# Kernel optimization log

Measured on AMD Instinct MI355X. Metric: run time of the kernel, lower is better.

## Reference

```python
import jax, jax.numpy as jnp
import numpy as np

T, B = 16, 32
C, H, W = 3, 120, 160
NET, LSTM_H, AC_H, NACT = 512, 512, 512, 8
CONV_OUT = 64 * 11 * 16  # 11264, from 120x160 through k[8,4,3]/s[4,2,1]


def setup_inputs() -> dict:
    key = jax.random.key(0)
    ks = jax.random.split(key, 32)
    rn = lambda k, shape, s=0.05: jax.random.normal(k, shape, jnp.float32) * s
    return {
        "x": jax.random.normal(ks[0], (T * B, C, H, W), jnp.float32),
        "done": jax.random.randint(ks[1], (T * B,), 0, 2, jnp.int32),
        "h0": rn(ks[2], (1, B, LSTM_H), 1.0),
        "c0": rn(ks[3], (1, B, LSTM_H), 1.0),
        "w1": rn(ks[4], (32, C, 8, 8)), "b1": jnp.zeros((32,), jnp.float32),
        "w2": rn(ks[5], (64, 32, 4, 4)), "b2": jnp.zeros((64,), jnp.float32),
        "w3": rn(ks[6], (64, 64, 3, 3)), "b3": jnp.zeros((64,), jnp.float32),
        "fcW": rn(ks[7], (NET, CONV_OUT), 0.01), "fcb": jnp.zeros((NET,), jnp.float32),
        "Wih": rn(ks[8], (4 * LSTM_H, NET)), "Whh": rn(ks[9], (4 * LSTM_H, LSTM_H)),
        "bih": jnp.zeros((4 * LSTM_H,), jnp.float32), "bhh": jnp.zeros((4 * LSTM_H,), jnp.float32),
        "A1": rn(ks[10], (AC_H, LSTM_H)), "Ab1": jnp.zeros((AC_H,), jnp.float32),
        "A2": rn(ks[11], (NACT, AC_H)), "Ab2": jnp.zeros((NACT,), jnp.float32),
        "C1": rn(ks[12], (AC_H, LSTM_H)), "Cb1": jnp.zeros((AC_H,), jnp.float32),
        "C2": rn(ks[13], (1, AC_H)), "Cb2": jnp.zeros((1,), jnp.float32),
    }


DN = ("NCHW", "OIHW", "NCHW")


def _conv(x, w, b, s):
    y = jax.lax.conv_general_dilated(x, w, (s, s), "VALID", dimension_numbers=DN)
    return y + b[None, :, None, None]


def reference(x, done, h0, c0, w1, b1, w2, b2, w3, b3, fcW, fcb,
              Wih, Whh, bih, bhh, A1, Ab1, A2, Ab2, C1, Cb1, C2, Cb2):
    # CNN feature extractor
    h = jax.nn.relu(_conv(x, w1, b1, 4))
    h = jax.nn.relu(_conv(h, w2, b2, 2))
    h = jax.nn.relu(_conv(h, w3, b3, 1))
    h = h.reshape(h.shape[0], -1)                     # [T*B, CONV_OUT]
    h = jax.nn.leaky_relu(h @ fcW.T + fcb, 0.2)       # [T*B, NET]

    bsz = h0.shape[1]
    xs = h.reshape(-1, bsz, Wih.shape[1])             # [T, B, NET]
    d = done.astype(h.dtype).reshape(-1, bsz)         # [T, B]

    def step(carry, inp):
        hs, cs = carry
        xt, dt = inp
        m = (1.0 - dt)[:, None]                       # done-mask reset
        hs, cs = hs * m, cs * m
        g = xt @ Wih.T + bih + hs @ Whh.T + bhh       # [B, 4H], gate order i,f,g,o
        i, f, gg, o = jnp.split(g, 4, axis=-1)
        cs = jax.nn.sigmoid(f) * cs + jax.nn.sigmoid(i) * jnp.tanh(gg)
        hs = jax.nn.sigmoid(o) * jnp.tanh(cs)
        return (hs, cs), hs

    (hT, cT), outs = jax.lax.scan(step, (h0[0], c0[0]), (xs, d))
    nh = outs.reshape(-1, outs.shape[-1])             # [T*B, LSTM_H]

    a = jax.nn.leaky_relu(nh @ A1.T + Ab1, 0.01)
    logits = a @ A2.T + Ab2                           # [T*B, NACT]
    v = jax.nn.leaky_relu(nh @ C1.T + Cb1, 0.01)
    value = v @ C2.T + Cb2                            # [T*B, 1]
    return logits, value, hT[None], cT[None]
```

## Files before the change

### kernel.cpp

```cpp
#include <hip/hip_runtime.h>
#include <hip/hip_bf16.h>
#include <math.h>

using short8 = __attribute__((ext_vector_type(8))) short;
using f32x4  = __attribute__((ext_vector_type(4))) float;
typedef unsigned long long u64;

#define MFMA16(a, b, c) __builtin_amdgcn_mfma_f32_16x16x32_bf16(a, b, c, 0, 0, 0)

__device__ __forceinline__ short f2bs(float f) {
    __hip_bfloat16 h = __float2bfloat16(f);
    return __builtin_bit_cast(short, h);
}
__device__ __forceinline__ float bs2f(short s) {
    return __uint_as_float(((unsigned)(unsigned short)s) << 16);
}

__global__ void __launch_bounds__(256) k_megaprep(
        const float* __restrict__ w1, const float* __restrict__ w2,
        const float* __restrict__ w3, const float* __restrict__ fcW,
        const float* __restrict__ Wih, const float* __restrict__ Whh,
        const float* __restrict__ A1, const float* __restrict__ C1,
        const float* __restrict__ A2, const float* __restrict__ C2,
        const float* __restrict__ h0, const int* __restrict__ done,
        const float* __restrict__ bih, const float* __restrict__ bhh,
        const float* __restrict__ Ab1, const float* __restrict__ Cb1,
        short* __restrict__ wc1, short* __restrict__ wc2, short* __restrict__ wc3,
        short* __restrict__ fcwr, short* __restrict__ wihb, short* __restrict__ whhb,
        short* __restrict__ a1b, short* __restrict__ c1b, short* __restrict__ a2b,
        short* __restrict__ c2b, short* __restrict__ hm0,
        float* __restrict__ bias2, float* __restrict__ biasAC, unsigned* __restrict__ flags) {
    __shared__ short t[176 * 76];
    const int bid = blockIdx.x, tid = threadIdx.x;

    auto cvt4 = [&](const float* in, short* out, int i) {
        float4 v = *(const float4*)(in + i * 4);
        out[i * 4 + 0] = f2bs(v.x); out[i * 4 + 1] = f2bs(v.y);
        out[i * 4 + 2] = f2bs(v.z); out[i * 4 + 3] = f2bs(v.w);
    };

    if (bid < 512) {
        int r = bid;
        for (int it = 0; it < 11; ++it) {
            int c4 = it * 256 + tid;
            float4 v = *(const float4*)(fcW + (size_t)r * 11264 + c4 * 4);
            int c = c4 * 4;
            int oc = c / 176, pix = c % 176;
            t[(pix + 0) * 76 + oc] = f2bs(v.x);
            t[(pix + 1) * 76 + oc] = f2bs(v.y);
            t[(pix + 2) * 76 + oc] = f2bs(v.z);
            t[(pix + 3) * 76 + oc] = f2bs(v.w);
        }
        __syncthreads();
        for (int it = 0; it < 6; ++it) {
            int j8 = it * 256 + tid;
            if (j8 < 1408) {
                int j = j8 * 8, pix = j >> 6, oc0 = j & 63;
                const short* tp = &t[pix * 76 + oc0];
                short8 v;
                ((uint2*)&v)[0] = *(const uint2*)tp;
                ((uint2*)&v)[1] = *(const uint2*)(tp + 4);
                *(short8*)&fcwr[(size_t)r * 11264 + j] = v;
            }
        }
    } else if (bid < 1536) {
        cvt4(Wih, wihb, (bid - 512) * 256 + tid);
    } else if (bid < 2560) {
        cvt4(Whh, whhb, (bid - 1536) * 256 + tid);
    } else if (bid < 2816) {
        cvt4(A1, a1b, (bid - 2560) * 256 + tid);
    } else if (bid < 3072) {
        cvt4(C1, c1b, (bid - 2816) * 256 + tid);
    } else if (bid < 3078) {
        cvt4(w1, wc1, (bid - 3072) * 256 + tid);
    } else if (bid < 3206) {
        int i = (bid - 3078) * 256 + tid;
        int oc = i >> 9, col = i & 511;
        int kh = col >> 7, kw = (col >> 5) & 3, ic = col & 31;
        wc2[i] = f2bs(w2[((oc * 32 + ic) * 4 + kh) * 4 + kw]);
    } else if (bid < 3350) {
        int i = (bid - 3206) * 256 + tid;
        int oc = i / 576, col = i % 576;
        int kh = col / 192, r = col % 192, kw = r >> 6, ic = r & 63;
        wc3[i] = f2bs(w3[((oc * 64 + ic) * 3 + kh) * 3 + kw]);
    } else if (bid < 3354) {
        cvt4(A2, a2b, (bid - 3350) * 256 + tid);
    } else if (bid < 3355) {
        if (tid < 128) cvt4(C2, c2b, tid);
    } else if (bid < 3419) {
        int i = (bid - 3355) * 256 + tid;
        float m = 1.f - (float)done[i >> 9];
        hm0[i] = f2bs(h0[i] * m);
    } else if (bid < 3427) {
        int i = (bid - 3419) * 256 + tid;
        bias2[i] = bih[i] + bhh[i];
    } else if (bid < 3431) {
        int i = (bid - 3427) * 256 + tid;
        biasAC[i] = (i < 512) ? Ab1[i] : Cb1[i - 512];
    } else {
        if (tid < 16) flags[tid] = 0u;
    }
}

__global__ void __launch_bounds__(256) k_conv1_v4(const float* __restrict__ x,
                                                  const short* __restrict__ Wc,
                                                  const float* __restrict__ bias,
                                                  short* __restrict__ y) {
    __shared__ short ct[4][512];
    const int tid = threadIdx.x;
    const int w = tid >> 6, l = tid & 63;
    const int lr = l & 15, lg = l >> 4;
    short8 bf[6][2];
#pragma unroll
    for (int ks = 0; ks < 6; ++ks)
#pragma unroll
        for (int nf = 0; nf < 2; ++nf)
            bf[ks][nf] = *(const short8*)&Wc[(nf * 16 + lr) * 192 + ks * 32 + lg * 8];
    const float bc0 = bias[lr], bc1 = bias[16 + lr];
    const int t0 = blockIdx.x * 16 + w * 4;

    auto mkbase = [&](int t) -> const float* {
        unsigned m = (unsigned)(t * 16 + lr);
        unsigned n = m / 1131u, pix = m % 1131u;
        unsigned oh = pix / 39u, ow = pix - oh * 39u;
        return x + (size_t)n * 57600 + (oh * 4) * 160 + ow * 4;
    };

    float4 fA[6][2], fB[6][2];
    {
        const float* base = mkbase(t0);
#pragma unroll
        for (int ks = 0; ks < 6; ++ks) {
            int ic = ks >> 1, kh = (ks & 1) * 4 + lg;
            const float* ap = base + ic * 19200 + kh * 160;
            fA[ks][0] = *(const float4*)ap;
            fA[ks][1] = *(const float4*)(ap + 4);
        }
    }
#pragma unroll
    for (int i = 0; i < 4; ++i) {
        const int t = t0 + i;
        if (i < 3) {
            const float* nb = mkbase(t + 1);
#pragma unroll
            for (int ks = 0; ks < 6; ++ks) {
                int ic = ks >> 1, kh = (ks & 1) * 4 + lg;
                const float* ap = nb + ic * 19200 + kh * 160;
                fB[ks][0] = *(const float4*)ap;
                fB[ks][1] = *(const float4*)(ap + 4);
            }
        }
        f32x4 acc[2] = {};
#pragma unroll
        for (int ks = 0; ks < 6; ++ks) {
            short8 a;
            a[0] = f2bs(fA[ks][0].x); a[1] = f2bs(fA[ks][0].y);
            a[2] = f2bs(fA[ks][0].z); a[3] = f2bs(fA[ks][0].w);
            a[4] = f2bs(fA[ks][1].x); a[5] = f2bs(fA[ks][1].y);
            a[6] = f2bs(fA[ks][1].z); a[7] = f2bs(fA[ks][1].w);
            acc[0] = MFMA16(a, bf[ks][0], acc[0]);
            acc[1] = MFMA16(a, bf[ks][1], acc[1]);
        }
#pragma unroll
        for (int j = 0; j < 4; ++j) {
            ct[w][(lg * 4 + j) * 32 + lr] = f2bs(fmaxf(acc[0][j] + bc0, 0.f));
            ct[w][(lg * 4 + j) * 32 + 16 + lr] = f2bs(fmaxf(acc[1][j] + bc1, 0.f));
        }
        asm volatile("s_waitcnt lgkmcnt(0)" ::: "memory");
        int row = l >> 2, c8 = (l & 3) * 8;
        short8 v = *(const short8*)&ct[w][row * 32 + c8];
        *(short8*)&y[((size_t)t * 16 + row) * 32 + c8] = v;
        asm volatile("s_waitcnt lgkmcnt(0)" ::: "memory");
        if (i < 3) {
#pragma unroll
            for (int ks = 0; ks < 6; ++ks) {
                fA[ks][0] = fB[ks][0];
                fA[ks][1] = fB[ks][1];
            }
        }
    }
}

__global__ void __launch_bounds__(256) k_conv23(const short* __restrict__ a1,
                                                const short* __restrict__ Wc2,
                                                const float* __restrict__ b2,
                                                const short* __restrict__ Wc3,
                                                const float* __restrict__ b3,
                                                short* __restrict__ y3) {
    __shared__ short img1[36192];
    __shared__ short img2[14976];
    __shared__ short ct[2][1024];
    const int n = blockIdx.x, tid = threadIdx.x;
    const int w = tid >> 6, l = tid & 63, lr = l & 15, lg = l >> 4;
    const int par = w >> 1, nfh = w & 1;

    {
        short8 bfg[16][2];
#pragma unroll
        for (int ks = 0; ks < 16; ++ks)
#pragma unroll
            for (int q2 = 0; q2 < 2; ++q2)
                bfg[ks][q2] = *(const short8*)&Wc2[(nfh * 32 + q2 * 16 + lr) * 512 + ks * 32 + lg * 8];
        float bc[2] = {b2[nfh * 32 + lr], b2[nfh * 32 + 16 + lr]};
        const short* src = a1 + (size_t)n * 36192;
        for (int it = 0; it < 18; ++it) {
            int i8 = it * 256 + tid;
            if (i8 < 4524) {
                short8 v = *(const short8*)(src + i8 * 8);
                int b = i8 * 16;
                b ^= ((b >> 7) & 7) << 4;
                *(short8*)((char*)img1 + b) = v;
            }
        }
        __syncthreads();
        for (int t = par; t < 16; t += 2) {
            int p = t * 16 + lr;
            int pc = p < 234 ? p : 233;
            int oh = pc / 18, ow = pc - oh * 18;
            int base = (oh * 2 * 39 + ow * 2) * 64 + lg * 16;
            f32x4 acc[2] = {};
#pragma unroll
            for (int ks = 0; ks < 16; ++ks) {
                int kh = ks >> 2, kw = ks & 3;
                int b = base + (kh * 39 + kw) * 64;
                b ^= ((b >> 7) & 7) << 4;
                short8 a = *(const short8*)((const char*)img1 + b);
                acc[0] = MFMA16(a, bfg[ks][0], acc[0]);
                acc[1] = MFMA16(a, bfg[ks][1], acc[1]);
            }
#pragma unroll
            for (int q2 = 0; q2 < 2; ++q2)
#pragma unroll
                for (int j = 0; j < 4; ++j)
                    ct[par][(lg * 4 + j) * 64 + nfh * 32 + q2 * 16 + lr] =
                        f2bs(fmaxf(acc[q2][j] + bc[q2], 0.f));
            __syncthreads();
            int li = nfh * 64 + l;
            int row = li >> 3, c8 = (li & 7) * 8;
            short8 v = *(const short8*)&ct[par][row * 64 + c8];
            int pg = t * 16 + row;
            if (pg < 234) {
                int b = (pg * 64 + c8) * 2;
                b ^= ((b >> 7) & 7) << 4;
                *(short8*)((char*)img2 + b) = v;
            }
            __syncthreads();
        }
    }
    __syncthreads();

    {
        short8 bfg[18][2];
#pragma unroll
        for (int ks = 0; ks < 18; ++ks)
#pragma unroll
            for (int q2 = 0; q2 < 2; ++q2)
                bfg[ks][q2] = *(const short8*)&Wc3[(nfh * 32 + q2 * 16 + lr) * 576 + ks * 32 + lg * 8];
        float bc[2] = {b3[nfh * 32 + lr], b3[nfh * 32 + 16 + lr]};
        for (int t = par; t < 12; t += 2) {
            int p = t * 16 + lr;
            int pc = p < 176 ? p : 175;
            int oh = pc >> 4, ow = pc & 15;
            int base = (oh * 18 + ow) * 128 + lg * 16;
            f32x4 acc[2] = {};
#pragma unroll
            for (int ks = 0; ks < 18; ++ks) {
                int kh = ks / 6, r6 = ks % 6, kw = r6 >> 1, ich = r6 & 1;
                int b = base + (kh * 18 + kw) * 128 + ich * 64;
                b ^= ((b >> 7) & 7) << 4;
                short8 a = *(const short8*)((const char*)img2 + b);
                acc[0] = MFMA16(a, bfg[ks][0], acc[0]);
                acc[1] = MFMA16(a, bfg[ks][1], acc[1]);
            }
#pragma unroll
            for (int q2 = 0; q2 < 2; ++q2)
#pragma unroll
                for (int j = 0; j < 4; ++j)
                    ct[par][(lg * 4 + j) * 64 + nfh * 32 + q2 * 16 + lr] =
                        f2bs(fmaxf(acc[q2][j] + bc[q2], 0.f));
            __syncthreads();
            int li = nfh * 64 + l;
            int row = li >> 3, c8 = (li & 7) * 8;
            short8 v = *(const short8*)&ct[par][row * 64 + c8];
            int pg = t * 16 + row;
            if (pg < 176)
                *(short8*)&y3[((size_t)n * 176 + pg) * 64 + c8] = v;
            __syncthreads();
        }
    }
}

__global__ void k_gemm_mfma(const short* __restrict__ A, const short* __restrict__ W,
                            float* __restrict__ part, int M, int N, int K, int kPerSplit) {
    __shared__ short As[2][64 * 40];
    __shared__ short Ws[2][64 * 40];
    const int tid = threadIdx.x;
    const int m0 = blockIdx.y * 64, n0 = blockIdx.x * 64;
    const int k0s = blockIdx.z * kPerSplit, k0e = k0s + kPerSplit;
    const int w = tid >> 6, l = tid & 63;
    const int wr = w >> 1, wc = w & 1;
    const int sr = tid >> 2, sc = tid & 3;
    const int lr = l & 15, lg = l >> 4;
    f32x4 acc[2][2] = {};
    for (int k0 = k0s; k0 < k0e; k0 += 64) {
        short8 av0 = *(const short8*)(A + (size_t)(m0 + sr) * K + k0 + sc * 8);
        short8 av1 = *(const short8*)(A + (size_t)(m0 + sr) * K + k0 + 32 + sc * 8);
        short8 wv0 = *(const short8*)(W + (size_t)(n0 + sr) * K + k0 + sc * 8);
        short8 wv1 = *(const short8*)(W + (size_t)(n0 + sr) * K + k0 + 32 + sc * 8);
        __syncthreads();
        *(short8*)&As[0][sr * 40 + sc * 8] = av0;
        *(short8*)&As[1][sr * 40 + sc * 8] = av1;
        *(short8*)&Ws[0][sr * 40 + sc * 8] = wv0;
        *(short8*)&Ws[1][sr * 40 + sc * 8] = wv1;
        __syncthreads();
        int cb = lg * 8;
#pragma unroll
        for (int h = 0; h < 2; ++h) {
            short8 a0 = *(const short8*)&As[h][(wr * 32 + lr) * 40 + cb];
            short8 a1 = *(const short8*)&As[h][(wr * 32 + 16 + lr) * 40 + cb];
            short8 b0 = *(const short8*)&Ws[h][(wc * 32 + lr) * 40 + cb];
            short8 b1 = *(const short8*)&Ws[h][(wc * 32 + 16 + lr) * 40 + cb];
            acc[0][0] = MFMA16(a0, b0, acc[0][0]);
            acc[0][1] = MFMA16(a0, b1, acc[0][1]);
            acc[1][0] = MFMA16(a1, b0, acc[1][0]);
            acc[1][1] = MFMA16(a1, b1, acc[1][1]);
        }
    }
    float* pp = part + (size_t)blockIdx.z * M * N;
#pragma unroll
    for (int mi = 0; mi < 2; ++mi)
#pragma unroll
        for (int ni = 0; ni < 2; ++ni)
#pragma unroll
            for (int j = 0; j < 4; ++j) {
                int row = m0 + wr * 32 + mi * 16 + lg * 4 + j;
                int col = n0 + wc * 32 + ni * 16 + lr;
                pp[(size_t)row * N + col] = acc[mi][ni][j];
            }
}

__global__ void k_epilogue(const float* __restrict__ part, const float* __restrict__ bias,
                           short* __restrict__ out_b, float* __restrict__ out_f,
                           int MN, int N, int S, float slope) {
    int i = (blockIdx.x * 256 + threadIdx.x) * 4;
    if (i >= MN) return;
    float4 v = *(const float4*)(part + i);
    for (int s = 1; s < S; ++s) {
        float4 p = *(const float4*)(part + (size_t)s * MN + i);
        v.x += p.x; v.y += p.y; v.z += p.z; v.w += p.w;
    }
    float4 b = *(const float4*)(bias + (i % N));
    v.x += b.x; v.y += b.y; v.z += b.z; v.w += b.w;
    v.x = (v.x >= 0.f) ? v.x : v.x * slope;
    v.y = (v.y >= 0.f) ? v.y : v.y * slope;
    v.z = (v.z >= 0.f) ? v.z : v.z * slope;
    v.w = (v.w >= 0.f) ? v.w : v.w * slope;
    if (out_b) {
        out_b[i + 0] = f2bs(v.x); out_b[i + 1] = f2bs(v.y);
        out_b[i + 2] = f2bs(v.z); out_b[i + 3] = f2bs(v.w);
    }
    if (out_f) *(float4*)(out_f + i) = v;
}

__global__ void k_gemm_bias(const short* __restrict__ A, const short* __restrict__ W,
                            const float* __restrict__ bias, short* __restrict__ out_b,
                            float* __restrict__ out_f, int M, int N, int K, float slope) {
    __shared__ short As[2][64 * 40];
    __shared__ short Ws[2][64 * 40];
    const int tid = threadIdx.x;
    const int m0 = blockIdx.y * 64, n0 = blockIdx.x * 64;
    const int w = tid >> 6, l = tid & 63;
    const int wr = w >> 1, wc = w & 1;
    const int sr = tid >> 2, sc = tid & 3;
    const int lr = l & 15, lg = l >> 4;
    f32x4 acc[2][2] = {};
    for (int k0 = 0; k0 < K; k0 += 64) {
        short8 av0 = *(const short8*)(A + (size_t)(m0 + sr) * K + k0 + sc * 8);
        short8 av1 = *(const short8*)(A + (size_t)(m0 + sr) * K + k0 + 32 + sc * 8);
        short8 wv0 = *(const short8*)(W + (size_t)(n0 + sr) * K + k0 + sc * 8);
        short8 wv1 = *(const short8*)(W + (size_t)(n0 + sr) * K + k0 + 32 + sc * 8);
        __syncthreads();
        *(short8*)&As[0][sr * 40 + sc * 8] = av0;
        *(short8*)&As[1][sr * 40 + sc * 8] = av1;
        *(short8*)&Ws[0][sr * 40 + sc * 8] = wv0;
        *(short8*)&Ws[1][sr * 40 + sc * 8] = wv1;
        __syncthreads();
        int cb = lg * 8;
#pragma unroll
        for (int h = 0; h < 2; ++h) {
            short8 a0 = *(const short8*)&As[h][(wr * 32 + lr) * 40 + cb];
            short8 a1 = *(const short8*)&As[h][(wr * 32 + 16 + lr) * 40 + cb];
            short8 b0 = *(const short8*)&Ws[h][(wc * 32 + lr) * 40 + cb];
            short8 b1 = *(const short8*)&Ws[h][(wc * 32 + 16 + lr) * 40 + cb];
            acc[0][0] = MFMA16(a0, b0, acc[0][0]);
            acc[0][1] = MFMA16(a0, b1, acc[0][1]);
            acc[1][0] = MFMA16(a1, b0, acc[1][0]);
            acc[1][1] = MFMA16(a1, b1, acc[1][1]);
        }
    }
#pragma unroll
    for (int mi = 0; mi < 2; ++mi)
#pragma unroll
        for (int ni = 0; ni < 2; ++ni)
#pragma unroll
            for (int j = 0; j < 4; ++j) {
                int row = m0 + wr * 32 + mi * 16 + lg * 4 + j;
                int col = n0 + wc * 32 + ni * 16 + lr;
                float v = acc[mi][ni][j] + bias[col];
                v = (v >= 0.f) ? v : v * slope;
                if (out_f) out_f[(size_t)row * N + col] = v;
                else       out_b[(size_t)row * N + col] = f2bs(v);
            }
}

__global__ void __launch_bounds__(1024) k_lstm_all4(
        const float* __restrict__ P, const short* __restrict__ Whhb,
        const int* __restrict__ done, u64* __restrict__ hq0, u64* __restrict__ hq1,
        const float* __restrict__ c0, short* __restrict__ nh,
        float* __restrict__ outH, float* __restrict__ outC, unsigned* __restrict__ flags) {
    __shared__ short hs[32 * 520];
    __shared__ float gb[4 * 32 * 33];
    __shared__ short ch[32 * 33];
    const int b = blockIdx.x;
    const int tid = threadIdx.x;
    const int w = tid >> 6, l = tid & 63, lr = l & 15, lg = l >> 4;
    const int mt = w & 1, nt = w >> 1;
    const int r = nt * 16 + lr;
    const int gate = r >> 5, ul = r & 31;
    const int G = gate * 512 + b * 32 + ul;
    short8 bfg[16];
    const short* wrow = Whhb + (size_t)G * 512;
#pragma unroll
    for (int ks = 0; ks < 16; ++ks) bfg[ks] = *(const short8*)(wrow + ks * 32 + lg * 8);
    const int cu = tid >> 5, cb = tid & 31;
    float cr = c0[cb * 512 + b * 32 + cu];
    const int pb = tid >> 3;
    unsigned dmC = 0, dmP = 0;
#pragma unroll
    for (int q = 0; q < 16; ++q) {
        dmC |= (done[q * 32 + cb] ? 1u : 0u) << q;
        dmP |= (done[q * 32 + pb] ? 1u : 0u) << q;
    }
    float pr[4];
#pragma unroll
    for (int j = 0; j < 4; ++j)
        pr[j] = P[(size_t)(mt * 16 + lg * 4 + j) * 2048 + G];

    for (int t = 0; t < 16; ++t) {
        const u64* hin = (t & 1) ? hq1 : hq0;
        u64* hout      = (t & 1) ? hq0 : hq1;
        if (t > 0) {
            if (tid < 16) {
                while (__hip_atomic_load(flags + tid, __ATOMIC_RELAXED,
                                         __HIP_MEMORY_SCOPE_AGENT) < (unsigned)t)
                    __builtin_amdgcn_s_sleep(1);
            }
            __syncthreads();
        }
#pragma unroll
        for (int it = 0; it < 4; ++it) {
            int i = it * 1024 + tid;
            u64 g = __hip_atomic_load(hin + i, __ATOMIC_RELAXED, __HIP_MEMORY_SCOPE_AGENT);
            *(u64*)&hs[(i >> 7) * 520 + (i & 127) * 4] = g;
        }
        __syncthreads();
        f32x4 acc = {};
#pragma unroll
        for (int ks = 0; ks < 16; ++ks) {
            short8 a = *(const short8*)&hs[(mt * 16 + lr) * 520 + ks * 32 + lg * 8];
            acc = MFMA16(a, bfg[ks], acc);
        }
#pragma unroll
        for (int j = 0; j < 4; ++j)
            gb[gate * 1056 + ul * 33 + (mt * 16 + lg * 4 + j)] = acc[j] + pr[j];
        __syncthreads();
        {
            float gi = gb[0 * 1056 + cu * 33 + cb];
            float gf = gb[1 * 1056 + cu * 33 + cb];
            float gg = gb[2 * 1056 + cu * 33 + cb];
            float go = gb[3 * 1056 + cu * 33 + cb];
            float m = ((dmC >> t) & 1u) ? 0.f : 1.f;
            float ig = 1.f / (1.f + expf(-gi));
            float fg = 1.f / (1.f + expf(-gf));
            float gt = tanhf(gg);
            float og = 1.f / (1.f + expf(-go));
            float cn = fg * (cr * m) + ig * gt;
            float hn = og * tanhf(cn);
            cr = cn;
            ch[cu * 33 + cb] = f2bs(hn);
            if (t == 15) {
                outH[cb * 512 + b * 32 + cu] = hn;
                outC[cb * 512 + b * 32 + cu] = cn;
            }
        }
        __syncthreads();
        if (t < 15) {
            if (tid < 256) {
                int bb3 = tid >> 3, uq = (tid & 7) * 4;
                u64 q = 0;
                if (!((dmP >> (t + 1)) & 1u)) {
                    unsigned lo = ((unsigned)(unsigned short)ch[uq * 33 + bb3]) |
                                  (((unsigned)(unsigned short)ch[(uq + 1) * 33 + bb3]) << 16);
                    unsigned hi = ((unsigned)(unsigned short)ch[(uq + 2) * 33 + bb3]) |
                                  (((unsigned)(unsigned short)ch[(uq + 3) * 33 + bb3]) << 16);
                    q = (u64)lo | ((u64)hi << 32);
                }
                __hip_atomic_store(hout + bb3 * 128 + b * 8 + (tid & 7), q,
                                   __ATOMIC_RELAXED, __HIP_MEMORY_SCOPE_AGENT);
            }
            asm volatile("s_waitcnt vmcnt(0)" ::: "memory");
            __syncthreads();
            if (tid == 0)
                __hip_atomic_store(flags + b, (unsigned)(t + 1),
                                   __ATOMIC_RELAXED, __HIP_MEMORY_SCOPE_AGENT);
        }
        if (tid < 512) {
            int bb2 = tid >> 4, up = (tid & 15) * 2;
            unsigned pkv = ((unsigned)(unsigned short)ch[up * 33 + bb2]) |
                           (((unsigned)(unsigned short)ch[(up + 1) * 33 + bb2]) << 16);
            *(unsigned*)&nh[(size_t)(t * 32 + bb2) * 512 + b * 32 + up] = pkv;
        }
        int tp = (t < 15) ? t + 1 : 15;
#pragma unroll
        for (int j = 0; j < 4; ++j)
            pr[j] = P[(size_t)(tp * 32 + mt * 16 + lg * 4 + j) * 2048 + G];
    }
}

__global__ void k_heads(const short* __restrict__ aAC,
                        const short* __restrict__ A2b, const float* __restrict__ Ab2,
                        const short* __restrict__ C2b, const float* __restrict__ Cb2,
                        float* __restrict__ out) {
    int idx = blockIdx.x * 4 + (threadIdx.x >> 6);
    int l = threadIdx.x & 63;
    if (idx >= 4608) return;
    int row = idx / 9, col = idx % 9;
    const short* act = aAC + (size_t)row * 1024 + (col < 8 ? 0 : 512);
    const short* wr  = (col < 8) ? (A2b + (size_t)col * 512) : C2b;
    short8 a = *(const short8*)(act + l * 8);
    short8 wv = *(const short8*)(wr + l * 8);
    float s = 0.f;
#pragma unroll
    for (int q = 0; q < 8; ++q) s += bs2f(a[q]) * bs2f(wv[q]);
#pragma unroll
    for (int off = 32; off > 0; off >>= 1) s += __shfl_xor(s, off, 64);
    if (l == 0) {
        if (col < 8) out[row * 8 + col] = s + Ab2[col];
        else out[4096 + row] = s + Cb2[0];
    }
}


extern "C" void kernel_launch(void* const* d_in, const int* in_sizes, int n_in,
                              void* d_out, int out_size, void* d_ws, size_t ws_size,
                              hipStream_t stream) {
    (void)in_sizes; (void)n_in; (void)out_size; (void)ws_size;
    const float* x    = (const float*)d_in[0];
    const int*   done = (const int*)  d_in[1];
    const float* h0   = (const float*)d_in[2];
    const float* c0   = (const float*)d_in[3];
    const float* w1   = (const float*)d_in[4];
    const float* b1   = (const float*)d_in[5];
    const float* w2   = (const float*)d_in[6];
    const float* b2   = (const float*)d_in[7];
    const float* w3   = (const float*)d_in[8];
    const float* b3   = (const float*)d_in[9];
    const float* fcW  = (const float*)d_in[10];
    const float* fcb  = (const float*)d_in[11];
    const float* Wih  = (const float*)d_in[12];
    const float* Whh  = (const float*)d_in[13];
    const float* bih  = (const float*)d_in[14];
    const float* bhh  = (const float*)d_in[15];
    const float* A1   = (const float*)d_in[16];
    const float* Ab1  = (const float*)d_in[17];
    const float* A2   = (const float*)d_in[18];
    const float* Ab2  = (const float*)d_in[19];
    const float* C1   = (const float*)d_in[20];
    const float* Cb1  = (const float*)d_in[21];
    const float* C2   = (const float*)d_in[22];
    const float* Cb2  = (const float*)d_in[23];
    float* out = (float*)d_out;

    char* wsp = (char*)d_ws;
    auto alloc = [&](size_t bytes) {
        char* p = wsp; wsp += (bytes + 255) & ~(size_t)255; return p;
    };
    short* a1s  = (short*)alloc(18530304ull * 2);
    short* a3s  = (short*)alloc(5767168ull * 2);
    short* hfc  = (short*)alloc(262144ull * 2);
    float* P    = (float*)alloc(1048576ull * 4);
    short* whhb = (short*)alloc(1048576ull * 2);
    u64*   hq0  = (u64*)  alloc(16384ull * 2);
    u64*   hq1  = (u64*)  alloc(16384ull * 2);
    short* nh   = (short*)alloc(262144ull * 2);
    short* aAC  = (short*)alloc(524288ull * 2);
    float* part = (float*)alloc(2097152ull * 4);
    short* wc1  = (short*)alloc(6144ull * 2);
    short* wc2  = (short*)alloc(32768ull * 2);
    short* wc3  = (short*)alloc(36864ull * 2);
    short* fcwr = (short*)alloc(5767168ull * 2);
    short* wihb = (short*)alloc(1048576ull * 2);
    short* a1b  = (short*)alloc(262144ull * 2);
    short* c1b  = (short*)alloc(262144ull * 2);
    short* a2b  = (short*)alloc(4096ull * 2);
    short* c2b  = (short*)alloc(512ull * 2);
    float* bias2  = (float*)alloc(2048ull * 4);
    float* biasAC = (float*)alloc(1024ull * 4);
    unsigned* flags = (unsigned*)alloc(256);

    k_megaprep<<<3432, 256, 0, stream>>>(w1, w2, w3, fcW, Wih, Whh, A1, C1, A2, C2,
                                         h0, done, bih, bhh, Ab1, Cb1,
                                         wc1, wc2, wc3, fcwr, wihb, whhb,
                                         a1b, c1b, a2b, c2b, (short*)hq0,
                                         bias2, biasAC, flags);

    k_conv1_v4<<<2262, 256, 0, stream>>>(x, wc1, b1, a1s);
    k_conv23<<<512, 256, 0, stream>>>(a1s, wc2, b2, wc3, b3, a3s);

    k_gemm_mfma<<<dim3(8, 8, 8), 256, 0, stream>>>(a3s, fcwr, part, 512, 512, 11264, 1408);
    k_epilogue<<<256, 256, 0, stream>>>(part, fcb, hfc, nullptr, 262144, 512, 8, 0.2f);

    k_gemm_bias<<<dim3(32, 8), 256, 0, stream>>>(hfc, wihb, bias2, nullptr, P,
                                                 512, 2048, 512, 1.0f);

    k_lstm_all4<<<16, 1024, 0, stream>>>(P, whhb, done, hq0, hq1, c0, nh,
                                         out + 4608, out + 20992, flags);

    k_gemm_bias<<<dim3(16, 8), 256, 0, stream>>>(nh, a1b, biasAC, aAC, nullptr,
                                                 512, 1024, 512, 0.01f);
    k_heads<<<1152, 256, 0, stream>>>(aAC, a2b, Ab2, c2b, Cb2, out);
}
```

Measured before the change: 215.4 us.

## Fuse conv1 into conv2/3 kernel, writing conv1 output directly to LDS

Merges the conv1 kernel into the conv2/conv3 kernel so that each block computes one image's conv1 activations and stores them straight into the swizzled shared-memory image buffer. This removes the roughly 37 MB bf16 global write and read of the intermediate activation, plus one kernel launch. In exchange, conv1 parallelism drops from 2262 blocks to 512 blocks, with each wave looping over about 18 tiles, so latency hiding and occupancy for the input-bound conv1 stage may suffer.

Measured after the change: 194.3 us, median of 3. 9.8% less time.

```diff
diff --git a/kernel.cpp b/kernel.cpp
--- a/kernel.cpp
+++ b/kernel.cpp
@@ -102,99 +102,97 @@
     }
 }
 
-__global__ void __launch_bounds__(256) k_conv1_v4(const float* __restrict__ x,
-                                                  const short* __restrict__ Wc,
-                                                  const float* __restrict__ bias,
-                                                  short* __restrict__ y) {
-    __shared__ short ct[4][512];
-    const int tid = threadIdx.x;
-    const int w = tid >> 6, l = tid & 63;
-    const int lr = l & 15, lg = l >> 4;
-    short8 bf[6][2];
-#pragma unroll
-    for (int ks = 0; ks < 6; ++ks)
-#pragma unroll
-        for (int nf = 0; nf < 2; ++nf)
-            bf[ks][nf] = *(const short8*)&Wc[(nf * 16 + lr) * 192 + ks * 32 + lg * 8];
-    const float bc0 = bias[lr], bc1 = bias[16 + lr];
-    const int t0 = blockIdx.x * 16 + w * 4;
-
-    auto mkbase = [&](int t) -> const float* {
-        unsigned m = (unsigned)(t * 16 + lr);
-        unsigned n = m / 1131u, pix = m % 1131u;
-        unsigned oh = pix / 39u, ow = pix - oh * 39u;
-        return x + (size_t)n * 57600 + (oh * 4) * 160 + ow * 4;
-    };
-
-    float4 fA[6][2], fB[6][2];
-    {
-        const float* base = mkbase(t0);
-#pragma unroll
-        for (int ks = 0; ks < 6; ++ks) {
-            int ic = ks >> 1, kh = (ks & 1) * 4 + lg;
-            const float* ap = base + ic * 19200 + kh * 160;
-            fA[ks][0] = *(const float4*)ap;
-            fA[ks][1] = *(const float4*)(ap + 4);
-        }
-    }
-#pragma unroll
-    for (int i = 0; i < 4; ++i) {
-        const int t = t0 + i;
-        if (i < 3) {
-            const float* nb = mkbase(t + 1);
-#pragma unroll
-            for (int ks = 0; ks < 6; ++ks) {
-                int ic = ks >> 1, kh = (ks & 1) * 4 + lg;
-                const float* ap = nb + ic * 19200 + kh * 160;
-                fB[ks][0] = *(const float4*)ap;
-                fB[ks][1] = *(const float4*)(ap + 4);
-            }
-        }
-        f32x4 acc[2] = {};
-#pragma unroll
-        for (int ks = 0; ks < 6; ++ks) {
-            short8 a;
-            a[0] = f2bs(fA[ks][0].x); a[1] = f2bs(fA[ks][0].y);
-            a[2] = f2bs(fA[ks][0].z); a[3] = f2bs(fA[ks][0].w);
-            a[4] = f2bs(fA[ks][1].x); a[5] = f2bs(fA[ks][1].y);
-            a[6] = f2bs(fA[ks][1].z); a[7] = f2bs(fA[ks][1].w);
-            acc[0] = MFMA16(a, bf[ks][0], acc[0]);
-            acc[1] = MFMA16(a, bf[ks][1], acc[1]);
-        }
-#pragma unroll
-        for (int j = 0; j < 4; ++j) {
-            ct[w][(lg * 4 + j) * 32 + lr] = f2bs(fmaxf(acc[0][j] + bc0, 0.f));
-            ct[w][(lg * 4 + j) * 32 + 16 + lr] = f2bs(fmaxf(acc[1][j] + bc1, 0.f));
-        }
-        asm volatile("s_waitcnt lgkmcnt(0)" ::: "memory");
-        int row = l >> 2, c8 = (l & 3) * 8;
-        short8 v = *(const short8*)&ct[w][row * 32 + c8];
-        *(short8*)&y[((size_t)t * 16 + row) * 32 + c8] = v;
-        asm volatile("s_waitcnt lgkmcnt(0)" ::: "memory");
-        if (i < 3) {
-#pragma unroll
-            for (int ks = 0; ks < 6; ++ks) {
-                fA[ks][0] = fB[ks][0];
-                fA[ks][1] = fB[ks][1];
-            }
-        }
-    }
-}
-
-__global__ void __launch_bounds__(256) k_conv23(const short* __restrict__ a1,
-                                                const short* __restrict__ Wc2,
-                                                const float* __restrict__ b2,
-                                                const short* __restrict__ Wc3,
-                                                const float* __restrict__ b3,
-                                                short* __restrict__ y3) {
+__global__ void __launch_bounds__(256) k_conv123(
+        const float* __restrict__ x,   const short* __restrict__ Wc1,
+        const float* __restrict__ b1,
+        const short* __restrict__ Wc2, const float* __restrict__ b2,
+        const short* __restrict__ Wc3, const float* __restrict__ b3,
+        short* __restrict__ y3) {
     __shared__ short img1[36192];
     __shared__ short img2[14976];
-    __shared__ short ct[2][1024];
+    __shared__ short ct[2048];
     const int n = blockIdx.x, tid = threadIdx.x;
     const int w = tid >> 6, l = tid & 63, lr = l & 15, lg = l >> 4;
     const int par = w >> 1, nfh = w & 1;
 
     {
+        short8 bf[6][2];
+#pragma unroll
+        for (int ks = 0; ks < 6; ++ks)
+#pragma unroll
+            for (int nf = 0; nf < 2; ++nf)
+                bf[ks][nf] = *(const short8*)&Wc1[(nf * 16 + lr) * 192 + ks * 32 + lg * 8];
+        const float bc0 = b1[lr], bc1 = b1[16 + lr];
+        const float* xb = x + (size_t)n * 57600;
+        auto tileBase = [&](int tt) -> const float* {
+            int p = tt * 16 + lr; if (p > 1130) p = 1130;
+            int oh = p / 39, ow = p - oh * 39;
+            return xb + (oh * 4) * 160 + ow * 4;
+        };
+        const int ntiles = (w == 3) ? 17 : 18;
+        float4 fA[6][2], fB[6][2];
+        {
+            const float* base = tileBase(w);
+#pragma unroll
+            for (int ks = 0; ks < 6; ++ks) {
+                int ic = ks >> 1, kh = (ks & 1) * 4 + lg;
+                const float* ap = base + ic * 19200 + kh * 160;
+                fA[ks][0] = *(const float4*)ap;
+                fA[ks][1] = *(const float4*)(ap + 4);
+            }
+        }
+        for (int i = 0; i < ntiles; ++i) {
+            const int tt = i * 4 + w;
+            if (i + 1 < ntiles) {
+                const float* nb = tileBase(tt + 4);
+#pragma unroll
+                for (int ks = 0; ks < 6; ++ks) {
+                    int ic = ks >> 1, kh = (ks & 1) * 4 + lg;
+                    const float* ap = nb + ic * 19200 + kh * 160;
+                    fB[ks][0] = *(const float4*)ap;
+                    fB[ks][1] = *(const float4*)(ap + 4);
+                }
+            }
+            f32x4 acc[2] = {};
+#pragma unroll
+            for (int ks = 0; ks < 6; ++ks) {
+                short8 a;
+                a[0] = f2bs(fA[ks][0].x); a[1] = f2bs(fA[ks][0].y);
+                a[2] = f2bs(fA[ks][0].z); a[3] = f2bs(fA[ks][0].w);
+                a[4] = f2bs(fA[ks][1].x); a[5] = f2bs(fA[ks][1].y);
+                a[6] = f2bs(fA[ks][1].z); a[7] = f2bs(fA[ks][1].w);
+                acc[0] = MFMA16(a, bf[ks][0], acc[0]);
+                acc[1] = MFMA16(a, bf[ks][1], acc[1]);
+            }
+#pragma unroll
+            for (int j = 0; j < 4; ++j) {
+                ct[w * 512 + (lg * 4 + j) * 32 + lr] = f2bs(fmaxf(acc[0][j] + bc0, 0.f));
+                ct[w * 512 + (lg * 4 + j) * 32 + 16 + lr] = f2bs(fmaxf(acc[1][j] + bc1, 0.f));
+            }
+            asm volatile("s_waitcnt lgkmcnt(0)" ::: "memory");
+            {
+                int row = l >> 2, c8 = (l & 3) * 8;
+                int pg = tt * 16 + row;
+                if (pg < 1131) {
+                    short8 v = *(const short8*)&ct[w * 512 + row * 32 + c8];
+                    int b = pg * 64 + c8 * 2;
+                    b ^= ((b >> 7) & 7) << 4;
+                    *(short8*)((char*)img1 + b) = v;
+                }
+            }
+            asm volatile("s_waitcnt lgkmcnt(0)" ::: "memory");
+            if (i + 1 < ntiles) {
+#pragma unroll
+                for (int ks = 0; ks < 6; ++ks) {
+                    fA[ks][0] = fB[ks][0];
+                    fA[ks][1] = fB[ks][1];
+                }
+            }
+        }
+    }
+    __syncthreads();
+
+    {
         short8 bfg[16][2];
 #pragma unroll
         for (int ks = 0; ks < 16; ++ks)
@@ -202,17 +200,6 @@
             for (int q2 = 0; q2 < 2; ++q2)
                 bfg[ks][q2] = *(const short8*)&Wc2[(nfh * 32 + q2 * 16 + lr) * 512 + ks * 32 + lg * 8];
         float bc[2] = {b2[nfh * 32 + lr], b2[nfh * 32 + 16 + lr]};
-        const short* src = a1 + (size_t)n * 36192;
-        for (int it = 0; it < 18; ++it) {
-            int i8 = it * 256 + tid;
-            if (i8 < 4524) {
-                short8 v = *(const short8*)(src + i8 * 8);
-                int b = i8 * 16;
-                b ^= ((b >> 7) & 7) << 4;
-                *(short8*)((char*)img1 + b) = v;
-            }
-        }
-        __syncthreads();
         for (int t = par; t < 16; t += 2) {
             int p = t * 16 + lr;
             int pc = p < 234 ? p : 233;
@@ -232,12 +219,12 @@
             for (int q2 = 0; q2 < 2; ++q2)
 #pragma unroll
                 for (int j = 0; j < 4; ++j)
-                    ct[par][(lg * 4 + j) * 64 + nfh * 32 + q2 * 16 + lr] =
+                    ct[par * 1024 + (lg * 4 + j) * 64 + nfh * 32 + q2 * 16 + lr] =
                         f2bs(fmaxf(acc[q2][j] + bc[q2], 0.f));
             __syncthreads();
             int li = nfh * 64 + l;
             int row = li >> 3, c8 = (li & 7) * 8;
-            short8 v = *(const short8*)&ct[par][row * 64 + c8];
+            short8 v = *(const short8*)&ct[par * 1024 + row * 64 + c8];
             int pg = t * 16 + row;
             if (pg < 234) {
                 int b = (pg * 64 + c8) * 2;
@@ -276,12 +263,12 @@
             for (int q2 = 0; q2 < 2; ++q2)
 #pragma unroll
                 for (int j = 0; j < 4; ++j)
-                    ct[par][(lg * 4 + j) * 64 + nfh * 32 + q2 * 16 + lr] =
+                    ct[par * 1024 + (lg * 4 + j) * 64 + nfh * 32 + q2 * 16 + lr] =
                         f2bs(fmaxf(acc[q2][j] + bc[q2], 0.f));
             __syncthreads();
             int li = nfh * 64 + l;
             int row = li >> 3, c8 = (li & 7) * 8;
-            short8 v = *(const short8*)&ct[par][row * 64 + c8];
+            short8 v = *(const short8*)&ct[par * 1024 + row * 64 + c8];
             int pg = t * 16 + row;
             if (pg < 176)
                 *(short8*)&y3[((size_t)n * 176 + pg) * 64 + c8] = v;
@@ -585,7 +572,6 @@
     auto alloc = [&](size_t bytes) {
         char* p = wsp; wsp += (bytes + 255) & ~(size_t)255; return p;
     };
-    short* a1s  = (short*)alloc(18530304ull * 2);
     short* a3s  = (short*)alloc(5767168ull * 2);
     short* hfc  = (short*)alloc(262144ull * 2);
     float* P    = (float*)alloc(1048576ull * 4);
@@ -614,8 +600,7 @@
                                          a1b, c1b, a2b, c2b, (short*)hq0,
                                          bias2, biasAC, flags);
 
-    k_conv1_v4<<<2262, 256, 0, stream>>>(x, wc1, b1, a1s);
-    k_conv23<<<512, 256, 0, stream>>>(a1s, wc2, b2, wc3, b3, a3s);
+    k_conv123<<<512, 256, 0, stream>>>(x, wc1, b1, wc2, b2, wc3, b3, a3s);
 
     k_gemm_mfma<<<dim3(8, 8, 8), 256, 0, stream>>>(a3s, fcwr, part, 512, 512, 11264, 1408);
     k_epilogue<<<256, 256, 0, stream>>>(part, fcb, hfc, nullptr, 262144, 512, 8, 0.2f);
```
